# Kernel tuning notes

Measured on AMD Instinct MI355X. Metric: run time of the kernel, lower is better.

Reference implementation:

```python
import jax, jax.numpy as jnp
import numpy as np

NUM_EMBEDDINGS = 1024
EMBEDDING_DIM = 256
COMMITMENT_COST = 0.25
B, D, T = 32, 256, 2048


def setup_inputs() -> dict:
    key = jax.random.key(0)
    k1, k2 = jax.random.split(key)
    inputs = jax.random.normal(k1, (B, D, T), dtype=jnp.float32)
    # nn.Embedding weight init: uniform(-1/K, 1/K)
    embeddings = jax.random.uniform(
        k2, (NUM_EMBEDDINGS, EMBEDDING_DIM), dtype=jnp.float32,
        minval=-1.0 / NUM_EMBEDDINGS, maxval=1.0 / NUM_EMBEDDINGS)
    return {"inputs": inputs, "embeddings": embeddings}


def reference(inputs, embeddings):
    # [B, D, T] -> [B, T, D]
    x = jnp.transpose(inputs, (0, 2, 1))
    Bs, Ts, Ds = x.shape
    flat = x.reshape(-1, Ds)  # [N, D]
    # squared L2 distances to each codebook entry: [N, K]
    distances = (jnp.sum(flat ** 2, axis=1, keepdims=True)
                 + jnp.sum(embeddings ** 2, axis=1)
                 - 2.0 * flat @ embeddings.T)
    encoding_indices = jnp.argmin(distances, axis=1)  # [N]
    # gather codebook rows (equivalent to one-hot @ embeddings)
    quantized = jnp.take(embeddings, encoding_indices, axis=0).reshape(x.shape)
    e_latent_loss = jnp.mean((jax.lax.stop_gradient(quantized) - x) ** 2)
    q_latent_loss = jnp.mean((quantized - jax.lax.stop_gradient(x)) ** 2)
    loss = q_latent_loss + COMMITMENT_COST * e_latent_loss
    # straight-through estimator
    quantized = x + jax.lax.stop_gradient(quantized - x)
    quantized = jnp.transpose(quantized, (0, 2, 1))  # back to [B, D, T]
    return quantized, loss, encoding_indices.reshape(Bs, Ts)
```

## Files before the change

### kernel.cpp

```cpp
#include <hip/hip_runtime.h>
#include <math.h>

#define K_CODES 1024
#define DIM 256
#define BB 32
#define TT 2048
#define NROWS (BB * TT)
#define QN (BB * DIM * TT)
#define LOSS_OFF QN
#define IDX_OFF (QN + 1)

#define WS_E2 0
#define WS_SX 1024
#define WS_LOSS (1024 + NROWS)

__device__ __forceinline__ float pw128_sq(const float* p, int stride) {
    float r[8];
#pragma unroll
    for (int j = 0; j < 8; ++j) {
        float v = p[j * stride];
        r[j] = __fmul_rn(v, v);
    }
#pragma unroll
    for (int i = 8; i < 128; i += 8) {
#pragma unroll
        for (int j = 0; j < 8; ++j) {
            float v = p[(i + j) * stride];
            r[j] = __fadd_rn(r[j], __fmul_rn(v, v));
        }
    }
    return __fadd_rn(__fadd_rn(__fadd_rn(r[0], r[1]), __fadd_rn(r[2], r[3])),
                     __fadd_rn(__fadd_rn(r[4], r[5]), __fadd_rn(r[6], r[7])));
}

__device__ __forceinline__ float pw256_sq(const float* p, int stride) {
    return __fadd_rn(pw128_sq(p, stride), pw128_sq(p + 128 * stride, stride));
}

__global__ void k_prep_e2(const float* __restrict__ emb, float* __restrict__ ws) {
    int k = blockIdx.x * 256 + threadIdx.x;
    if (k == 0) ws[WS_LOSS] = 0.0f;
    if (k < K_CODES) ws[WS_E2 + k] = pw256_sq(emb + (size_t)k * DIM, 1);
}

__global__ void k_prep_sx(const float* __restrict__ in, float* __restrict__ ws) {
    int row = blockIdx.x * 256 + threadIdx.x;
    int b = row >> 11;
    int t = row & (TT - 1);
    ws[WS_SX + row] = pw256_sq(in + (size_t)b * (DIM * TT) + t, TT);
}

__launch_bounds__(256, 2)
__global__ void k_main(const float* __restrict__ in, const float* __restrict__ emb,
                       const float* __restrict__ ws, float* __restrict__ wloss,
                       float* __restrict__ out) {
    __shared__ float smem[8192];
    __shared__ int idx_lds[128];
    float* xs = smem;
    float* es = smem + 4096;

    const int tid = threadIdx.x;
    const int tx = tid & 15;
    const int ty = tid >> 4;
    const int row0 = blockIdx.x * 128;
    const int b = row0 >> 11;
    const int t0 = row0 & (TT - 1);
    const float* xbase = in + (size_t)b * (DIM * TT) + t0;

    float sxr[8];
#pragma unroll
    for (int i = 0; i < 8; ++i) sxr[i] = ws[WS_SX + row0 + 8 * ty + i];

    float bestd[8];
    int bestidx[8];
#pragma unroll
    for (int i = 0; i < 8; ++i) { bestd[i] = INFINITY; bestidx[i] = 0; }

    const int lr = tid & 127;
    const int lh = tid >> 7;

    for (int cc = 0; cc < 8; ++cc) {
        const int cbase = cc * 128;
        float acc[8][8];
#pragma unroll
        for (int i = 0; i < 8; ++i)
#pragma unroll
            for (int j = 0; j < 8; ++j) acc[i][j] = 0.0f;

        for (int dc = 0; dc < 8; ++dc) {
            const int d0 = dc * 32;
            __syncthreads();
#pragma unroll
            for (int it = 0; it < 4; ++it) {
                int c4 = lh + 2 * it;
                float v0 = xbase[(size_t)(d0 + 4 * c4 + 0) * TT + lr];
                float v1 = xbase[(size_t)(d0 + 4 * c4 + 1) * TT + lr];
                float v2 = xbase[(size_t)(d0 + 4 * c4 + 2) * TT + lr];
                float v3 = xbase[(size_t)(d0 + 4 * c4 + 3) * TT + lr];
                int cs = c4 ^ ((lr >> 3) & 7);
                *(float4*)&xs[lr * 32 + cs * 4] = make_float4(v0, v1, v2, v3);
            }
#pragma unroll
            for (int it = 0; it < 4; ++it) {
                int s = tid + 256 * it;
                int code = s >> 3;
                int c4 = s & 7;
                float4 v = *(const float4*)&emb[(size_t)(cbase + code) * DIM + d0 + c4 * 4];
                int cs = c4 ^ ((code >> 3) & 7);
                *(float4*)&es[code * 32 + cs * 4] = v;
            }
            __syncthreads();
#pragma unroll
            for (int c4 = 0; c4 < 8; ++c4) {
                float4 xv[8], ev[8];
                const int xc = (c4 ^ (ty & 7)) * 4;
                const int ec = (c4 ^ (tx & 7)) * 4;
#pragma unroll
                for (int i = 0; i < 8; ++i) xv[i] = *(const float4*)&xs[(8 * ty + i) * 32 + xc];
#pragma unroll
                for (int j = 0; j < 8; ++j) ev[j] = *(const float4*)&es[(8 * tx + j) * 32 + ec];
#pragma unroll
                for (int i = 0; i < 8; ++i)
#pragma unroll
                    for (int j = 0; j < 8; ++j) {
                        float a = acc[i][j];
                        a = __fmaf_rn(xv[i].x, ev[j].x, a);
                        a = __fmaf_rn(xv[i].y, ev[j].y, a);
                        a = __fmaf_rn(xv[i].z, ev[j].z, a);
                        a = __fmaf_rn(xv[i].w, ev[j].w, a);
                        acc[i][j] = a;
                    }
            }
        }
#pragma unroll
        for (int j = 0; j < 8; ++j) {
            const int code = cbase + 8 * tx + j;
            const float e2 = ws[WS_E2 + code];
#pragma unroll
            for (int i = 0; i < 8; ++i) {
                float dist = __fsub_rn(__fadd_rn(sxr[i], e2), __fmul_rn(2.0f, acc[i][j]));
                if (dist < bestd[i]) { bestd[i] = dist; bestidx[i] = code; }
            }
        }
    }

    __syncthreads();
    float* rd = smem;
    int* ri = (int*)(smem + 2048);
#pragma unroll
    for (int i = 0; i < 8; ++i) {
        rd[(8 * ty + i) * 16 + tx] = bestd[i];
        ri[(8 * ty + i) * 16 + tx] = bestidx[i];
    }
    __syncthreads();
    if (tid < 128) {
        float bd = rd[tid * 16];
        int bi = ri[tid * 16];
#pragma unroll
        for (int x = 1; x < 16; ++x) {
            float d = rd[tid * 16 + x];
            int ix = ri[tid * 16 + x];
            if (d < bd || (d == bd && ix < bi)) { bd = d; bi = ix; }
        }
        idx_lds[tid] = bi;
        out[IDX_OFF + b * TT + t0 + tid] = (float)bi;
    }
    __syncthreads();

    float lsum = 0.0f;
    float* q = smem;
    const int qr = tid >> 3;
    const int qf = tid & 7;
    const int er_ = tid & 127;
    const int ed_ = tid >> 7;
    for (int dc = 0; dc < 8; ++dc) {
        const int d0 = dc * 32;
        __syncthreads();
#pragma unroll
        for (int it = 0; it < 4; ++it) {
            int r = qr + 32 * it;
            float4 v = *(const float4*)&emb[(size_t)idx_lds[r] * DIM + d0 + qf * 4];
            float* dst = &q[r * 37 + qf * 4];
            dst[0] = v.x; dst[1] = v.y; dst[2] = v.z; dst[3] = v.w;
        }
        __syncthreads();
#pragma unroll
        for (int k = 0; k < 16; ++k) {
            int dd = ed_ + 2 * k;
            float qq = q[er_ * 37 + dd];
            size_t gaddr = (size_t)b * (DIM * TT) + (size_t)(d0 + dd) * TT + t0 + er_;
            float xx = in[gaddr];
            out[gaddr] = qq;
            float df = __fsub_rn(qq, xx);
            lsum = __fmaf_rn(df, df, lsum);
        }
    }
#pragma unroll
    for (int off = 32; off > 0; off >>= 1) lsum += __shfl_down(lsum, off, 64);
    if ((tid & 63) == 0) atomicAdd(wloss, lsum);
}

__global__ void k_loss(const float* __restrict__ wloss, float* __restrict__ out) {
    out[LOSS_OFF] = 1.25f * wloss[0] / 16777216.0f;
}

extern "C" void kernel_launch(void* const* d_in, const int* in_sizes, int n_in,
                              void* d_out, int out_size, void* d_ws, size_t ws_size,
                              hipStream_t stream) {
    const float* in = (const float*)d_in[0];
    const float* emb = (const float*)d_in[1];
    float* out = (float*)d_out;
    float* ws = (float*)d_ws;

    hipLaunchKernelGGL(k_prep_e2, dim3(4), dim3(256), 0, stream, emb, ws);
    hipLaunchKernelGGL(k_prep_sx, dim3(256), dim3(256), 0, stream, in, ws);
    hipLaunchKernelGGL(k_main, dim3(512), dim3(256), 0, stream, in, emb, ws,
                       ws + WS_LOSS, out);
    hipLaunchKernelGGL(k_loss, dim3(1), dim3(1), 0, stream, ws + WS_LOSS, out);
}
```

Baseline: 625.0 us.

## Split codebook search across two blocks and merge via 64-bit atomicMin

```diff
diff --git a/kernel.cpp b/kernel.cpp
--- a/kernel.cpp
+++ b/kernel.cpp
@@ -13,6 +13,7 @@
 #define WS_E2 0
 #define WS_SX 1024
 #define WS_LOSS (1024 + NROWS)
+#define WS_BEST (WS_LOSS + 2)
 
 __device__ __forceinline__ float pw128_sq(const float* p, int stride) {
     float r[8];
@@ -48,21 +49,23 @@
     int b = row >> 11;
     int t = row & (TT - 1);
     ws[WS_SX + row] = pw256_sq(in + (size_t)b * (DIM * TT) + t, TT);
-}
-
-__launch_bounds__(256, 2)
+    ((unsigned long long*)(ws + WS_BEST))[row] = 0xFFFFFFFFFFFFFFFFull;
+}
+
+__launch_bounds__(256, 4)
 __global__ void k_main(const float* __restrict__ in, const float* __restrict__ emb,
-                       const float* __restrict__ ws, float* __restrict__ wloss,
-                       float* __restrict__ out) {
+                       const float* __restrict__ ws,
+                       unsigned long long* __restrict__ best) {
     __shared__ float smem[8192];
-    __shared__ int idx_lds[128];
     float* xs = smem;
     float* es = smem + 4096;
 
     const int tid = threadIdx.x;
     const int tx = tid & 15;
     const int ty = tid >> 4;
-    const int row0 = blockIdx.x * 128;
+    const int rowTile = blockIdx.x >> 1;
+    const int ch = blockIdx.x & 1;
+    const int row0 = rowTile * 128;
     const int b = row0 >> 11;
     const int t0 = row0 & (TT - 1);
     const float* xbase = in + (size_t)b * (DIM * TT) + t0;
@@ -76,11 +79,11 @@
 #pragma unroll
     for (int i = 0; i < 8; ++i) { bestd[i] = INFINITY; bestidx[i] = 0; }
 
-    const int lr = tid & 127;
+    const int lr = ((tid & 7) << 3) | ((tid >> 3) & 7) | (tid & 64);
     const int lh = tid >> 7;
 
-    for (int cc = 0; cc < 8; ++cc) {
-        const int cbase = cc * 128;
+    for (int cc = 0; cc < 4; ++cc) {
+        const int cbase = ch * 512 + cc * 128;
         float acc[8][8];
 #pragma unroll
         for (int i = 0; i < 8; ++i)
@@ -162,13 +165,30 @@
             int ix = ri[tid * 16 + x];
             if (d < bd || (d == bd && ix < bi)) { bd = d; bi = ix; }
         }
+        unsigned long long key =
+            ((unsigned long long)__float_as_uint(bd) << 32) | (unsigned int)bi;
+        atomicMin(&best[row0 + tid], key);
+    }
+}
+
+__launch_bounds__(256, 4)
+__global__ void k_epi(const float* __restrict__ in, const float* __restrict__ emb,
+                      const unsigned long long* __restrict__ best,
+                      float* __restrict__ wloss, float* __restrict__ out) {
+    __shared__ float q[128 * 37];
+    __shared__ int idx_lds[128];
+    const int tid = threadIdx.x;
+    const int row0 = blockIdx.x * 128;
+    const int b = row0 >> 11;
+    const int t0 = row0 & (TT - 1);
+
+    if (tid < 128) {
+        int bi = (int)(unsigned int)(best[row0 + tid] & 0xFFFFFFFFull);
         idx_lds[tid] = bi;
         out[IDX_OFF + b * TT + t0 + tid] = (float)bi;
     }
-    __syncthreads();
 
     float lsum = 0.0f;
-    float* q = smem;
     const int qr = tid >> 3;
     const int qf = tid & 7;
     const int er_ = tid & 127;
@@ -211,10 +231,12 @@
     const float* emb = (const float*)d_in[1];
     float* out = (float*)d_out;
     float* ws = (float*)d_ws;
+    unsigned long long* best = (unsigned long long*)(ws + WS_BEST);
 
     hipLaunchKernelGGL(k_prep_e2, dim3(4), dim3(256), 0, stream, emb, ws);
     hipLaunchKernelGGL(k_prep_sx, dim3(256), dim3(256), 0, stream, in, ws);
-    hipLaunchKernelGGL(k_main, dim3(512), dim3(256), 0, stream, in, emb, ws,
+    hipLaunchKernelGGL(k_main, dim3(1024), dim3(256), 0, stream, in, emb, ws, best);
+    hipLaunchKernelGGL(k_epi, dim3(512), dim3(256), 0, stream, in, emb, best,
                        ws + WS_LOSS, out);
     hipLaunchKernelGGL(k_loss, dim3(1), dim3(1), 0, stream, ws + WS_LOSS, out);
 }
```

Result: slower. 783.0 us (+25.3%).
